# Kernel optimization log

Measured on AMD Instinct MI355X. Metric: run time of the kernel, lower is better.

Reference implementation:

```python
import jax, jax.numpy as jnp
import numpy as np

GROUPSIZE = 4      # g: multivariate group size (d = groupsize - 2)
NB_GROUPS = 48     # f: number of expert groups / filters
CHANNELS = 128     # c: signal channels fed to the L operator
SCALE = 0.999
SLOPE = 1.0        # model_params['scaling']
LAMB_INIT = 0.1
EPS_OMEGA_INIT = -2.0


def proj_l1(x):
    """Euclidean projection onto the unit l1 ball along axis 1. x: [B,G,F,H,W]."""
    ax = jnp.abs(x)
    s = -jnp.sort(-ax, axis=1)                      # descending |x|
    cssv = jnp.cumsum(s, axis=1) - 1.0
    G = x.shape[1]
    k = jnp.arange(1, G + 1, dtype=x.dtype).reshape(1, G, 1, 1, 1)
    cond = s * k > cssv
    rho = jnp.sum(cond, axis=1, keepdims=True)       # number of active coords
    theta = jnp.take_along_axis(cssv, rho - 1, axis=1) / rho.astype(x.dtype)
    theta = jnp.maximum(theta, 0.0)
    proj = jnp.sign(x) * jnp.maximum(ax - theta, 0.0)
    inside = jnp.sum(ax, axis=1, keepdims=True) <= 1.0
    return jnp.where(inside, x, proj)


def _forward(x_noisy, sigma, Q_param, taus_param, lamb, eps_omega,
             mu_w1, mu_b1, mu_w2, mu_b2, mu_w3, mu_b3, Wf, n_iter):
    lamb_e = jnp.exp(lamb)
    eps_e = jnp.exp(eps_omega)

    # --- Q normalization + spectral norms (cached once per forward) ---
    Q = Q_param / jnp.maximum(jnp.sum(jnp.abs(Q_param), axis=2, keepdims=True), 1.0)
    Q_norms = jnp.linalg.svd(Q, compute_uv=False)[:, 0].reshape(-1, 1, 1)  # [F,1,1]
    Q_eff = Q / Q_norms ** 2
    taus = jnp.exp(jax.nn.relu(taus_param))          # [1,1,F,1,1]

    # --- per-batch noise-adaptive scaling via small MLP ---
    h = jax.nn.relu((sigma * 20.0 - 2.0) @ mu_w1 + mu_b1)
    h = jax.nn.relu(h @ mu_w2 + mu_b2)
    h = h @ mu_w3 + mu_b3                            # [B,F]
    scaling = jax.nn.relu(h * 0.05 + sigma) * SLOPE + 1e-9
    scaling = scaling.reshape(-1, 1, scaling.shape[-1], 1, 1)  # [B,1,F,1,1]

    def moreau(x):
        g = proj_l1(x)
        cost = jnp.max(jnp.abs(x - g), axis=1) + 0.5 * jnp.sum(g * g, axis=1)
        cost = cost[:, None]                         # [B,1,F,H,W]
        g = g + eps_e * x
        cost = cost + eps_e * 0.5 * jnp.sqrt(jnp.sum(x * x, axis=1, keepdims=True))
        return g, cost

    def activation(x):
        gc, cc = moreau(x)
        # orient: scale * einsum('flg,bgfhw->blfhw', Q/Q_norms^2, x), then /taus
        y = SCALE * jnp.einsum('flg,bgfhw->blfhw', Q_eff, x) / taus
        gcc, ccc = moreau(y)
        # unorient: scale * einsum with Q^T  (Q^T[f,l,g] = Q[f,g,l])
        gcc = SCALE * jnp.einsum('fgl,bgfhw->blfhw', Q, gcc)
        ccc = Q_norms ** 2 * (taus * ccc)
        return lamb_e * (gc - gcc), lamb_e * (cc - ccc)

    def reconstruct(x):
        Lx = jnp.einsum('gfc,bchw->bgfhw', Wf, x) / scaling
        g, cost = activation(Lx)
        g = jnp.einsum('gfc,bgfhw->bchw', Wf, g * scaling)   # adjoint L^T
        cost = jnp.sum(cost * scaling ** 2, axis=(1, 2, 3, 4))
        g = (x - x_noisy + g) / (1.0 + lamb_e * (1.0 + eps_e))
        cost = cost + 0.5 * jnp.sum((x - x_noisy) ** 2, axis=(1, 2, 3))
        return g, cost

    def step(x, _):
        g, _c = reconstruct(x)
        return x - g, None

    x_final, _ = jax.lax.scan(jax.checkpoint(step), x_noisy, jnp.arange(n_iter))
    return x_final


def setup_inputs() -> dict:
    key = jax.random.key(0)
    ks = jax.random.split(key, 8)
    B, C, H, W = 2, CHANNELS, 128, 128
    F_, G = NB_GROUPS, GROUPSIZE
    x_noisy = jax.random.normal(ks[0], (B, C, H, W), jnp.float32)
    sigma = jax.random.uniform(ks[1], (B, 1), jnp.float32)
    Q_param = jax.random.uniform(ks[2], (F_, G, G), jnp.float32) - 0.5
    taus_param = (LAMB_INIT / 2.0) * jnp.ones((1, 1, F_, 1, 1), jnp.float32)
    lamb = jnp.float32(LAMB_INIT)
    eps_omega = jnp.float32(EPS_OMEGA_INIT)
    mu_w1 = jax.random.normal(ks[3], (1, F_), jnp.float32)
    mu_b1 = jnp.zeros((F_,), jnp.float32)
    mu_w2 = jax.random.normal(ks[4], (F_, F_), jnp.float32) / np.float32(np.sqrt(F_))
    mu_b2 = jnp.zeros((F_,), jnp.float32)
    mu_w3 = jax.random.normal(ks[5], (F_, F_), jnp.float32) / np.float32(np.sqrt(F_))
    mu_b3 = jnp.zeros((F_,), jnp.float32)
    Wf = jax.random.normal(ks[6], (G, F_, C), jnp.float32) / np.float32(np.sqrt(C))
    return dict(x_noisy=x_noisy, sigma=sigma, Q_param=Q_param, taus_param=taus_param,
                lamb=lamb, eps_omega=eps_omega, mu_w1=mu_w1, mu_b1=mu_b1,
                mu_w2=mu_w2, mu_b2=mu_b2, mu_w3=mu_w3, mu_b3=mu_b3, Wf=Wf, n_iter=10)


def reference(x_noisy, sigma, Q_param, taus_param, lamb, eps_omega,
              mu_w1, mu_b1, mu_w2, mu_b2, mu_w3, mu_b3, Wf, n_iter):
    return _forward(x_noisy, sigma, Q_param, taus_param, lamb, eps_omega,
                    mu_w1, mu_b1, mu_w2, mu_b2, mu_w3, mu_b3, Wf, n_iter)
```

## Files before the change

kernel.cpp:

```cpp
#include <hip/hip_runtime.h>
#include <math.h>

#define F_ 48
#define C_ 128
#define HW 16384
#define SCALE_C 0.999f
#define TPB 256

typedef __attribute__((ext_vector_type(8))) short short8;
typedef __attribute__((ext_vector_type(4))) float floatx4;
typedef __attribute__((ext_vector_type(8))) _Float16 half8;
typedef __attribute__((ext_vector_type(4))) _Float16 half4;

#define P1_U 0
#define P2_U 98304
#define QEQN_F 98304
#define MISC_F (QEQN_F + 1536)
#define SINV_F (MISC_F + 2)
#define SLAM_F (SINV_F + 96)

#define XS 152
#define AS 104
#define QS 36

__device__ __forceinline__ unsigned short f2bf(float f) {
    unsigned u = __float_as_uint(f);
    unsigned r = u + 0x7fffu + ((u >> 16) & 1u);
    return (unsigned short)(r >> 16);
}
__device__ __forceinline__ float bf2f(unsigned short h) {
    return __uint_as_float(((unsigned)h) << 16);
}

__global__ void setup_math(const float* __restrict__ sigma,
                           const float* __restrict__ Qp,
                           const float* __restrict__ taus_p,
                           const float* __restrict__ lamb,
                           const float* __restrict__ eps_om,
                           const float* __restrict__ mw1, const float* __restrict__ mb1,
                           const float* __restrict__ mw2, const float* __restrict__ mb2,
                           const float* __restrict__ mw3, const float* __restrict__ mb3,
                           float* __restrict__ wsf)
{
    const int tid = threadIdx.x;
    if (tid < F_) {
        const int f = tid;
        float Qm[4][4];
        for (int g = 0; g < 4; ++g) {
            float s = 0.f;
            for (int l = 0; l < 4; ++l) s += fabsf(Qp[f * 16 + g * 4 + l]);
            float d = fmaxf(s, 1.0f);
            for (int l = 0; l < 4; ++l) Qm[g][l] = Qp[f * 16 + g * 4 + l] / d;
        }
        double A[4][4];
        for (int i = 0; i < 4; ++i)
            for (int j = 0; j < 4; ++j) {
                double s = 0.0;
                for (int g = 0; g < 4; ++g) s += (double)Qm[g][i] * (double)Qm[g][j];
                A[i][j] = s;
            }
        double M[4][4];
        for (int i = 0; i < 4; ++i) for (int j = 0; j < 4; ++j) M[i][j] = A[i][j];
        for (int it = 0; it < 30; ++it) {
            double T[4][4]; double mx = 0.0;
            for (int i = 0; i < 4; ++i)
                for (int j = 0; j < 4; ++j) {
                    double s = 0.0;
                    for (int k = 0; k < 4; ++k) s += M[i][k] * M[k][j];
                    T[i][j] = s;
                    double a = fabs(s); if (a > mx) mx = a;
                }
            if (mx < 1e-300) break;
            double inv = 1.0 / mx;
            for (int i = 0; i < 4; ++i) for (int j = 0; j < 4; ++j) M[i][j] = T[i][j] * inv;
        }
        int jb = 0; double bn = -1.0;
        for (int j = 0; j < 4; ++j) {
            double nn = 0.0;
            for (int i = 0; i < 4; ++i) nn += M[i][j] * M[i][j];
            if (nn > bn) { bn = nn; jb = j; }
        }
        double v[4]; for (int i = 0; i < 4; ++i) v[i] = M[i][jb];
        double Av[4];
        for (int i = 0; i < 4; ++i) {
            double s = 0.0;
            for (int j = 0; j < 4; ++j) s += A[i][j] * v[j];
            Av[i] = s;
        }
        double vv = 0.0, vav = 0.0;
        for (int i = 0; i < 4; ++i) { vv += v[i] * v[i]; vav += v[i] * Av[i]; }
        float lamf = (float)((vv > 0.0) ? (vav / vv) : 0.0);
        float tau = expf(fmaxf(taus_p[f], 0.0f));
        float qsv = SCALE_C / tau;
        for (int l = 0; l < 4; ++l)
            for (int g = 0; g < 4; ++g)
                wsf[QEQN_F + f * 32 + l * 4 + g] = qsv * Qm[l][g] / lamf;
        for (int g = 0; g < 4; ++g)
            for (int l = 0; l < 4; ++l)
                wsf[QEQN_F + f * 32 + 16 + g * 4 + l] = SCALE_C * Qm[g][l];
    }
    if (tid >= 48 && tid < 50) {
        const int b = tid - 48;
        float lamb_e = expf(lamb[0]);
        float sg = sigma[b];
        float t = sg * 20.0f - 2.0f;
        float h1[F_], h2[F_];
        for (int j = 0; j < F_; ++j) h1[j] = fmaxf(t * mw1[j] + mb1[j], 0.0f);
        for (int j = 0; j < F_; ++j) {
            float s = mb2[j];
            for (int k = 0; k < F_; ++k) s += h1[k] * mw2[k * F_ + j];
            h2[j] = fmaxf(s, 0.0f);
        }
        for (int j = 0; j < F_; ++j) {
            float s = mb3[j];
            for (int k = 0; k < F_; ++k) s += h2[k] * mw3[k * F_ + j];
            float sc = fmaxf(s * 0.05f + sg, 0.0f) + 1e-9f;
            wsf[SINV_F + b * F_ + j] = 1.0f / sc;
            wsf[SLAM_F + b * F_ + j] = lamb_e * sc;
        }
    }
    if (tid == 50) {
        float lamb_e = expf(lamb[0]);
        float eps_e = expf(eps_om[0]);
        wsf[MISC_F + 0] = eps_e;
        wsf[MISC_F + 1] = 1.0f / (1.0f + lamb_e * (1.0f + eps_e));
    }
}

__global__ void setup_pack(const float* __restrict__ Wf, float* __restrict__ wsf)
{
    unsigned short* wsu = (unsigned short*)wsf;
    const int gtid = blockIdx.x * TPB + threadIdx.x;
    for (int i = gtid; i < 49152; i += gridDim.x * TPB) {
        if (i < 24576) {
            int j = i & 7, lane = (i >> 3) & 63;
            int t = i >> 9;
            int ks = t & 3, mt = t >> 2;
            int m = lane & 15, q = lane >> 4;
            int r = mt * 16 + m;
            int c = ks * 32 + q * 8 + j;
            int f = r >> 2, g = r & 3;
            float w = Wf[(g * F_ + f) * C_ + c];
            _Float16 hv = (_Float16)w;
            wsu[P1_U + ((mt * 4 + ks) * 64 + lane) * 8 + j] = *(unsigned short*)&hv;
        } else {
            int ii = i - 24576;
            int j = ii & 7, lane = (ii >> 3) & 63;
            int t = ii >> 9;
            int ks = t % 6, cmt = t / 6;
            int m = lane & 15, q = lane >> 4;
            int cch = cmt * 16 + m;
            int r = ks * 32 + q * 8 + j;
            int g = r & 3;
            int f = r >> 2;
            float w = Wf[(g * F_ + f) * C_ + cch];
            _Float16 hv = (_Float16)w;
            wsu[P2_U + ((cmt * 6 + ks) * 64 + lane) * 8 + j] = *(unsigned short*)&hv;
        }
    }
}

__device__ __forceinline__ void proj4(const float v[4], float o[4]) {
    float a0 = fabsf(v[0]), a1 = fabsf(v[1]), a2 = fabsf(v[2]), a3 = fabsf(v[3]);
    float sum = a0 + a1 + a2 + a3;
    float t0 = fmaxf(a0, a1), u0 = fminf(a0, a1);
    float t1 = fmaxf(a2, a3), u1 = fminf(a2, a3);
    float s0 = fmaxf(t0, t1), m0 = fminf(t0, t1);
    float m1 = fmaxf(u0, u1), s3 = fminf(u0, u1);
    float s1 = fmaxf(m1, m0), s2 = fminf(m1, m0);
    float c2 = s0 + s1, c3 = c2 + s2, c4 = c3 + s3;
    float th = s0 - 1.0f, rh = 1.0f;
    if (s1 * 2.0f > c2 - 1.0f) { th = c2 - 1.0f; rh = 2.0f; }
    if (s2 * 3.0f > c3 - 1.0f) { th = c3 - 1.0f; rh = 3.0f; }
    if (s3 * 4.0f > c4 - 1.0f) { th = c4 - 1.0f; rh = 4.0f; }
    float theta = fmaxf(th / rh, 0.0f);
    bool inside = (sum <= 1.0f);
#pragma unroll
    for (int g = 0; g < 4; ++g) {
        float ag = fabsf(v[g]);
        float pg = copysignf(fmaxf(ag - theta, 0.0f), v[g]);
        o[g] = inside ? v[g] : pg;
    }
}

__global__ __launch_bounds__(TPB, 4) void mfoe_main(
    const float* __restrict__ xnoisy,
    const float* __restrict__ wsf,
    float* __restrict__ out,
    const int* __restrict__ n_iter_p)
{
    __shared__ __align__(16) _Float16 sXF[32 * XS];
    __shared__ __align__(16) _Float16 sACT[32 * AS];
    __shared__ __align__(16) float sQ[F_ * QS];

    const int tid = threadIdx.x;
    const int lane = tid & 63;
    const int wv = __builtin_amdgcn_readfirstlane(tid >> 6);
    const int n = lane & 15;
    const int q = lane >> 4;
    const int blk = blockIdx.x;
    const int b = blk >> 9;
    const int pix0 = (blk & 511) << 5;

    const float* __restrict__ xin = xnoisy + b * (C_ * HW) + pix0;
    float* __restrict__ oimg = out + b * (C_ * HW) + pix0;
    const unsigned short* __restrict__ wsu = (const unsigned short*)wsf;
    const int niter = *n_iter_p;

    if (niter == 0) {
        for (int i = tid; i < C_ * 32; i += TPB) {
            int p = i & 31, c = i >> 5;
            oimg[c * HW + p] = xin[c * HW + p];
        }
        return;
    }

    for (int i = tid; i < C_ * 32; i += TPB) {
        int p = i & 31, c = i >> 5;
        sXF[p * XS + c] = (_Float16)xin[c * HW + p];
    }
    for (int i = tid; i < F_ * 32; i += TPB)
        sQ[(i >> 5) * QS + (i & 31)] = wsf[QEQN_F + i];
    for (int i = tid; i < F_; i += TPB) {
        sQ[i * QS + 32] = wsf[SINV_F + b * F_ + i];
        sQ[i * QS + 33] = wsf[SLAM_F + b * F_ + i];
    }

    float xnr[16];
#pragma unroll
    for (int j = 0; j < 4; ++j) {
        int jw = wv * 4 + j, cmt = jw >> 1, nt = jw & 1;
        int p = nt * 16 + n;
#pragma unroll
        for (int reg = 0; reg < 4; ++reg)
            xnr[j * 4 + reg] = xin[(cmt * 16 + q * 4 + reg) * HW + p];
    }
    const float eps_e = wsf[MISC_F + 0];
    const float invden = wsf[MISC_F + 1];

    for (int it = 0; it < niter; ++it) {
        floatx4 acc2[4];
#pragma unroll
        for (int j = 0; j < 4; ++j) acc2[j] = (floatx4){0.f, 0.f, 0.f, 0.f};

#pragma unroll 1
        for (int h = 0; h < 2; ++h) {
            __syncthreads();
#pragma unroll 1
            for (int j = 0; j < 3; ++j) {
                int jw = wv * 3 + j, mtl = jw >> 1, nt = jw & 1;
                int mt = h * 6 + mtl;
                int p = nt * 16 + n;
                floatx4 acc = (floatx4){0.f, 0.f, 0.f, 0.f};
                const half8* aFp = (const half8*)(wsu + P1_U + (mt * 4) * 512 + lane * 8);
#pragma unroll
                for (int ks = 0; ks < 4; ++ks) {
                    half8 aF = aFp[ks * 64];
                    half8 bF = *(const half8*)&sXF[p * XS + ks * 32 + q * 8];
                    acc = __builtin_amdgcn_mfma_f32_16x16x32_f16(aF, bF, acc, 0, 0, 0);
                }
                int f = h * 24 + mtl * 4 + q;
                float qv[32];
#pragma unroll
                for (int k = 0; k < 8; ++k)
                    *(floatx4*)&qv[4 * k] = *(const floatx4*)&sQ[f * QS + 4 * k];
                float invs = sQ[f * QS + 32];
                float slam = sQ[f * QS + 33];
                float v[4] = {acc[0] * invs, acc[1] * invs, acc[2] * invs, acc[3] * invs};
                float pv[4]; proj4(v, pv);
                float y[4];
#pragma unroll
                for (int l = 0; l < 4; ++l)
                    y[l] = fmaf(qv[l * 4 + 0], v[0], fmaf(qv[l * 4 + 1], v[1],
                           fmaf(qv[l * 4 + 2], v[2], qv[l * 4 + 3] * v[3])));
                float py[4]; proj4(y, py);
                float m2[4];
#pragma unroll
                for (int g = 0; g < 4; ++g) m2[g] = fmaf(eps_e, y[g], py[g]);
                half4 av;
                {
                    float gcc0 = fmaf(qv[16 + 0], m2[0], fmaf(qv[16 + 4], m2[1],
                                 fmaf(qv[16 + 8], m2[2], qv[16 + 12] * m2[3])));
                    av[0] = (_Float16)((fmaf(eps_e, v[0], pv[0]) - gcc0) * slam);
                    float gcc1 = fmaf(qv[17 + 0], m2[0], fmaf(qv[17 + 4], m2[1],
                                 fmaf(qv[17 + 8], m2[2], qv[17 + 12] * m2[3])));
                    av[1] = (_Float16)((fmaf(eps_e, v[1], pv[1]) - gcc1) * slam);
                    float gcc2 = fmaf(qv[18 + 0], m2[0], fmaf(qv[18 + 4], m2[1],
                                 fmaf(qv[18 + 8], m2[2], qv[18 + 12] * m2[3])));
                    av[2] = (_Float16)((fmaf(eps_e, v[2], pv[2]) - gcc2) * slam);
                    float gcc3 = fmaf(qv[19 + 0], m2[0], fmaf(qv[19 + 4], m2[1],
                                 fmaf(qv[19 + 8], m2[2], qv[19 + 12] * m2[3])));
                    av[3] = (_Float16)((fmaf(eps_e, v[3], pv[3]) - gcc3) * slam);
                }
                *(half4*)&sACT[p * AS + mtl * 16 + q * 4] = av;
            }
            __syncthreads();
#pragma unroll
            for (int j = 0; j < 4; ++j) {
                int jw = wv * 4 + j, cmt = jw >> 1, nt = jw & 1;
                int p = nt * 16 + n;
                const half8* a2F = (const half8*)(wsu + P2_U + ((cmt * 6 + h * 3) * 64) * 8 + lane * 8);
                floatx4 a = acc2[j];
#pragma unroll
                for (int ksl = 0; ksl < 3; ++ksl) {
                    half8 aF = a2F[ksl * 64];
                    half8 bA = *(const half8*)&sACT[p * AS + ksl * 32 + q * 8];
                    a = __builtin_amdgcn_mfma_f32_16x16x32_f16(aF, bA, a, 0, 0, 0);
                }
                acc2[j] = a;
            }
        }
        const bool last = (it == niter - 1);
#pragma unroll
        for (int j = 0; j < 4; ++j) {
            int jw = wv * 4 + j, cmt = jw >> 1, nt = jw & 1;
            int p = nt * 16 + n;
            int cb = cmt * 16 + q * 4;
            half4 xo4 = *(const half4*)&sXF[p * XS + cb];
            float xo0 = (float)xo4[0];
            float xo1 = (float)xo4[1];
            float xo2 = (float)xo4[2];
            float xo3 = (float)xo4[3];
            float nx0 = xo0 - ((xo0 - xnr[j * 4 + 0]) + acc2[j][0]) * invden;
            float nx1 = xo1 - ((xo1 - xnr[j * 4 + 1]) + acc2[j][1]) * invden;
            float nx2 = xo2 - ((xo2 - xnr[j * 4 + 2]) + acc2[j][2]) * invden;
            float nx3 = xo3 - ((xo3 - xnr[j * 4 + 3]) + acc2[j][3]) * invden;
            if (last) {
                oimg[(cb + 0) * HW + p] = nx0;
                oimg[(cb + 1) * HW + p] = nx1;
                oimg[(cb + 2) * HW + p] = nx2;
                oimg[(cb + 3) * HW + p] = nx3;
            }
            half4 nx4;
            nx4[0] = (_Float16)nx0;
            nx4[1] = (_Float16)nx1;
            nx4[2] = (_Float16)nx2;
            nx4[3] = (_Float16)nx3;
            *(half4*)&sXF[p * XS + cb] = nx4;
        }
    }
}

extern "C" void kernel_launch(void* const* d_in, const int* in_sizes, int n_in,
                              void* d_out, int out_size, void* d_ws, size_t ws_size,
                              hipStream_t stream) {
    const float* x_noisy = (const float*)d_in[0];
    const float* sigma   = (const float*)d_in[1];
    const float* Qp      = (const float*)d_in[2];
    const float* taus_p  = (const float*)d_in[3];
    const float* lamb    = (const float*)d_in[4];
    const float* eps_om  = (const float*)d_in[5];
    const float* mw1     = (const float*)d_in[6];
    const float* mb1     = (const float*)d_in[7];
    const float* mw2     = (const float*)d_in[8];
    const float* mb2     = (const float*)d_in[9];
    const float* mw3     = (const float*)d_in[10];
    const float* mb3     = (const float*)d_in[11];
    const float* Wf      = (const float*)d_in[12];
    const int*   n_iter  = (const int*)d_in[13];
    float* out = (float*)d_out;
    float* ws  = (float*)d_ws;

    hipLaunchKernelGGL(setup_math, dim3(1), dim3(64), 0, stream,
                       sigma, Qp, taus_p, lamb, eps_om,
                       mw1, mb1, mw2, mb2, mw3, mb3, ws);
    hipLaunchKernelGGL(setup_pack, dim3(192), dim3(TPB), 0, stream, Wf, ws);
    hipLaunchKernelGGL(mfoe_main, dim3(1024), dim3(TPB), 0, stream,
                       x_noisy, ws, out, n_iter);
}
```

Before: 286.9 us.

## Use 512-thread blocks and drop the two-half split of the filter loop

The main kernel now runs 8 waves per block instead of 4. The full set of 48 filters' activations is computed in one pass into a wider shared activation buffer, instead of in two halves. The second GEMM then accumulates over all 6 K-steps at once, which removes one pair of barriers per iteration and gives each wave fewer output tiles. The cost is larger LDS use per block and more threads contending at each barrier, which may lower occupancy.

```diff
diff --git a/kernel.cpp b/kernel.cpp
--- a/kernel.cpp
+++ b/kernel.cpp
@@ -6,6 +6,7 @@
 #define HW 16384
 #define SCALE_C 0.999f
 #define TPB 256
+#define MTPB 512
 
 typedef __attribute__((ext_vector_type(8))) short short8;
 typedef __attribute__((ext_vector_type(4))) float floatx4;
@@ -20,7 +21,7 @@
 #define SLAM_F (SINV_F + 96)
 
 #define XS 152
-#define AS 104
+#define AS 200
 #define QS 36
 
 __device__ __forceinline__ unsigned short f2bf(float f) {
@@ -183,7 +184,7 @@
     }
 }
 
-__global__ __launch_bounds__(TPB, 4) void mfoe_main(
+__global__ __launch_bounds__(MTPB, 4) void mfoe_main(
     const float* __restrict__ xnoisy,
     const float* __restrict__ wsf,
     float* __restrict__ out,
@@ -208,28 +209,28 @@
     const int niter = *n_iter_p;
 
     if (niter == 0) {
-        for (int i = tid; i < C_ * 32; i += TPB) {
+        for (int i = tid; i < C_ * 32; i += MTPB) {
             int p = i & 31, c = i >> 5;
             oimg[c * HW + p] = xin[c * HW + p];
         }
         return;
     }
 
-    for (int i = tid; i < C_ * 32; i += TPB) {
+    for (int i = tid; i < C_ * 32; i += MTPB) {
         int p = i & 31, c = i >> 5;
         sXF[p * XS + c] = (_Float16)xin[c * HW + p];
     }
-    for (int i = tid; i < F_ * 32; i += TPB)
+    for (int i = tid; i < F_ * 32; i += MTPB)
         sQ[(i >> 5) * QS + (i & 31)] = wsf[QEQN_F + i];
-    for (int i = tid; i < F_; i += TPB) {
+    for (int i = tid; i < F_; i += MTPB) {
         sQ[i * QS + 32] = wsf[SINV_F + b * F_ + i];
         sQ[i * QS + 33] = wsf[SLAM_F + b * F_ + i];
     }
 
-    float xnr[16];
-#pragma unroll
-    for (int j = 0; j < 4; ++j) {
-        int jw = wv * 4 + j, cmt = jw >> 1, nt = jw & 1;
+    float xnr[8];
+#pragma unroll
+    for (int j = 0; j < 2; ++j) {
+        int jw = wv * 2 + j, cmt = jw >> 1, nt = jw & 1;
         int p = nt * 16 + n;
 #pragma unroll
         for (int reg = 0; reg < 4; ++reg)
@@ -239,81 +240,76 @@
     const float invden = wsf[MISC_F + 1];
 
     for (int it = 0; it < niter; ++it) {
-        floatx4 acc2[4];
-#pragma unroll
-        for (int j = 0; j < 4; ++j) acc2[j] = (floatx4){0.f, 0.f, 0.f, 0.f};
-
+        __syncthreads();
 #pragma unroll 1
-        for (int h = 0; h < 2; ++h) {
-            __syncthreads();
-#pragma unroll 1
-            for (int j = 0; j < 3; ++j) {
-                int jw = wv * 3 + j, mtl = jw >> 1, nt = jw & 1;
-                int mt = h * 6 + mtl;
-                int p = nt * 16 + n;
-                floatx4 acc = (floatx4){0.f, 0.f, 0.f, 0.f};
-                const half8* aFp = (const half8*)(wsu + P1_U + (mt * 4) * 512 + lane * 8);
-#pragma unroll
-                for (int ks = 0; ks < 4; ++ks) {
-                    half8 aF = aFp[ks * 64];
-                    half8 bF = *(const half8*)&sXF[p * XS + ks * 32 + q * 8];
-                    acc = __builtin_amdgcn_mfma_f32_16x16x32_f16(aF, bF, acc, 0, 0, 0);
-                }
-                int f = h * 24 + mtl * 4 + q;
-                float qv[32];
-#pragma unroll
-                for (int k = 0; k < 8; ++k)
-                    *(floatx4*)&qv[4 * k] = *(const floatx4*)&sQ[f * QS + 4 * k];
-                float invs = sQ[f * QS + 32];
-                float slam = sQ[f * QS + 33];
-                float v[4] = {acc[0] * invs, acc[1] * invs, acc[2] * invs, acc[3] * invs};
-                float pv[4]; proj4(v, pv);
-                float y[4];
-#pragma unroll
-                for (int l = 0; l < 4; ++l)
-                    y[l] = fmaf(qv[l * 4 + 0], v[0], fmaf(qv[l * 4 + 1], v[1],
-                           fmaf(qv[l * 4 + 2], v[2], qv[l * 4 + 3] * v[3])));
-                float py[4]; proj4(y, py);
-                float m2[4];
-#pragma unroll
-                for (int g = 0; g < 4; ++g) m2[g] = fmaf(eps_e, y[g], py[g]);
-                half4 av;
-                {
-                    float gcc0 = fmaf(qv[16 + 0], m2[0], fmaf(qv[16 + 4], m2[1],
-                                 fmaf(qv[16 + 8], m2[2], qv[16 + 12] * m2[3])));
-                    av[0] = (_Float16)((fmaf(eps_e, v[0], pv[0]) - gcc0) * slam);
-                    float gcc1 = fmaf(qv[17 + 0], m2[0], fmaf(qv[17 + 4], m2[1],
-                                 fmaf(qv[17 + 8], m2[2], qv[17 + 12] * m2[3])));
-                    av[1] = (_Float16)((fmaf(eps_e, v[1], pv[1]) - gcc1) * slam);
-                    float gcc2 = fmaf(qv[18 + 0], m2[0], fmaf(qv[18 + 4], m2[1],
-                                 fmaf(qv[18 + 8], m2[2], qv[18 + 12] * m2[3])));
-                    av[2] = (_Float16)((fmaf(eps_e, v[2], pv[2]) - gcc2) * slam);
-                    float gcc3 = fmaf(qv[19 + 0], m2[0], fmaf(qv[19 + 4], m2[1],
-                                 fmaf(qv[19 + 8], m2[2], qv[19 + 12] * m2[3])));
-                    av[3] = (_Float16)((fmaf(eps_e, v[3], pv[3]) - gcc3) * slam);
-                }
-                *(half4*)&sACT[p * AS + mtl * 16 + q * 4] = av;
-            }
-            __syncthreads();
-#pragma unroll
-            for (int j = 0; j < 4; ++j) {
-                int jw = wv * 4 + j, cmt = jw >> 1, nt = jw & 1;
-                int p = nt * 16 + n;
-                const half8* a2F = (const half8*)(wsu + P2_U + ((cmt * 6 + h * 3) * 64) * 8 + lane * 8);
-                floatx4 a = acc2[j];
-#pragma unroll
-                for (int ksl = 0; ksl < 3; ++ksl) {
-                    half8 aF = a2F[ksl * 64];
-                    half8 bA = *(const half8*)&sACT[p * AS + ksl * 32 + q * 8];
-                    a = __builtin_amdgcn_mfma_f32_16x16x32_f16(aF, bA, a, 0, 0, 0);
-                }
-                acc2[j] = a;
-            }
+        for (int j = 0; j < 3; ++j) {
+            int jw = wv * 3 + j, mt = jw >> 1, nt = jw & 1;
+            int p = nt * 16 + n;
+            floatx4 acc = (floatx4){0.f, 0.f, 0.f, 0.f};
+            const half8* aFp = (const half8*)(wsu + P1_U + (mt * 4) * 512 + lane * 8);
+#pragma unroll
+            for (int ks = 0; ks < 4; ++ks) {
+                half8 aF = aFp[ks * 64];
+                half8 bF = *(const half8*)&sXF[p * XS + ks * 32 + q * 8];
+                acc = __builtin_amdgcn_mfma_f32_16x16x32_f16(aF, bF, acc, 0, 0, 0);
+            }
+            int f = mt * 4 + q;
+            float qv[32];
+#pragma unroll
+            for (int k = 0; k < 8; ++k)
+                *(floatx4*)&qv[4 * k] = *(const floatx4*)&sQ[f * QS + 4 * k];
+            float invs = sQ[f * QS + 32];
+            float slam = sQ[f * QS + 33];
+            float v[4] = {acc[0] * invs, acc[1] * invs, acc[2] * invs, acc[3] * invs};
+            float pv[4]; proj4(v, pv);
+            float y[4];
+#pragma unroll
+            for (int l = 0; l < 4; ++l)
+                y[l] = fmaf(qv[l * 4 + 0], v[0], fmaf(qv[l * 4 + 1], v[1],
+                       fmaf(qv[l * 4 + 2], v[2], qv[l * 4 + 3] * v[3])));
+            float py[4]; proj4(y, py);
+            float m2[4];
+#pragma unroll
+            for (int g = 0; g < 4; ++g) m2[g] = fmaf(eps_e, y[g], py[g]);
+            half4 av;
+            {
+                float gcc0 = fmaf(qv[16 + 0], m2[0], fmaf(qv[16 + 4], m2[1],
+                             fmaf(qv[16 + 8], m2[2], qv[16 + 12] * m2[3])));
+                av[0] = (_Float16)((fmaf(eps_e, v[0], pv[0]) - gcc0) * slam);
+                float gcc1 = fmaf(qv[17 + 0], m2[0], fmaf(qv[17 + 4], m2[1],
+                             fmaf(qv[17 + 8], m2[2], qv[17 + 12] * m2[3])));
+                av[1] = (_Float16)((fmaf(eps_e, v[1], pv[1]) - gcc1) * slam);
+                float gcc2 = fmaf(qv[18 + 0], m2[0], fmaf(qv[18 + 4], m2[1],
+                             fmaf(qv[18 + 8], m2[2], qv[18 + 12] * m2[3])));
+                av[2] = (_Float16)((fmaf(eps_e, v[2], pv[2]) - gcc2) * slam);
+                float gcc3 = fmaf(qv[19 + 0], m2[0], fmaf(qv[19 + 4], m2[1],
+                             fmaf(qv[19 + 8], m2[2], qv[19 + 12] * m2[3])));
+                av[3] = (_Float16)((fmaf(eps_e, v[3], pv[3]) - gcc3) * slam);
+            }
+            *(half4*)&sACT[p * AS + mt * 16 + q * 4] = av;
+        }
+        __syncthreads();
+        floatx4 acc2[2];
+#pragma unroll
+        for (int j = 0; j < 2; ++j) acc2[j] = (floatx4){0.f, 0.f, 0.f, 0.f};
+#pragma unroll
+        for (int j = 0; j < 2; ++j) {
+            int jw = wv * 2 + j, cmt = jw >> 1, nt = jw & 1;
+            int p = nt * 16 + n;
+            const half8* a2F = (const half8*)(wsu + P2_U + ((cmt * 6) * 64) * 8 + lane * 8);
+            floatx4 a = acc2[j];
+#pragma unroll
+            for (int ks = 0; ks < 6; ++ks) {
+                half8 aF = a2F[ks * 64];
+                half8 bA = *(const half8*)&sACT[p * AS + ks * 32 + q * 8];
+                a = __builtin_amdgcn_mfma_f32_16x16x32_f16(aF, bA, a, 0, 0, 0);
+            }
+            acc2[j] = a;
         }
         const bool last = (it == niter - 1);
 #pragma unroll
-        for (int j = 0; j < 4; ++j) {
-            int jw = wv * 4 + j, cmt = jw >> 1, nt = jw & 1;
+        for (int j = 0; j < 2; ++j) {
+            int jw = wv * 2 + j, cmt = jw >> 1, nt = jw & 1;
             int p = nt * 16 + n;
             int cb = cmt * 16 + q * 4;
             half4 xo4 = *(const half4*)&sXF[p * XS + cb];
@@ -365,6 +361,6 @@
                        sigma, Qp, taus_p, lamb, eps_om,
                        mw1, mb1, mw2, mb2, mw3, mb3, ws);
     hipLaunchKernelGGL(setup_pack, dim3(192), dim3(TPB), 0, stream, Wf, ws);
-    hipLaunchKernelGGL(mfoe_main, dim3(1024), dim3(TPB), 0, stream,
+    hipLaunchKernelGGL(mfoe_main, dim3(1024), dim3(MTPB), 0, stream,
                        x_noisy, ws, out, n_iter);
 }
```

Measured after the change: 267.8 us. -6.7%, faster.
